# Kernel optimization log

Measured on AMD Instinct MI355X. Metric: run time of the kernel, lower is better.

Reference implementation:

```python
import jax, jax.numpy as jnp
import numpy as np

DENOM = 1.0 * (32 ** 0.5)  # temperature * map_rank**0.5
LN_EPS = 1e-5


def setup_inputs() -> dict:
    key = jax.random.key(0)
    ks = jax.random.split(key, 12)
    B, S, SC, MC, R, O = 4, 512, 128, 64, 32, 64
    sc = lambda *sh: 1.0 / np.sqrt(sh[0])
    return {
        "map_": jax.random.normal(ks[0], (B, MC, S, S), jnp.float32),
        "seq": jax.random.normal(ks[1], (B, S, SC), jnp.float32),
        "Wq": jax.random.normal(ks[2], (SC, R), jnp.float32) * sc(SC),
        "bq": jax.random.normal(ks[3], (R,), jnp.float32) * 0.01,
        "Wk": jax.random.normal(ks[4], (SC, R), jnp.float32) * sc(SC),
        "bk": jax.random.normal(ks[5], (R,), jnp.float32) * 0.01,
        "Wv": jax.random.normal(ks[6], (MC, MC), jnp.float32) * sc(MC),
        "bv": jax.random.normal(ks[7], (MC,), jnp.float32) * 0.01,
        "gamma": jnp.ones((MC,), jnp.float32),
        "beta": jnp.zeros((MC,), jnp.float32),
        "W1": jax.random.normal(ks[8], (MC, 4 * O), jnp.float32) * sc(MC),
        "b1": jax.random.normal(ks[9], (4 * O,), jnp.float32) * 0.01,
        "W2": jax.random.normal(ks[10], (4 * O, O), jnp.float32) * sc(4 * O),
        "b2": jax.random.normal(ks[11], (O,), jnp.float32) * 0.01,
    }


def _layernorm(x, gamma, beta):
    mu = jnp.mean(x, axis=-1, keepdims=True)
    var = jnp.mean(jnp.square(x - mu), axis=-1, keepdims=True)
    return (x - mu) * jax.lax.rsqrt(var + LN_EPS) * gamma + beta


def reference(map_, seq, Wq, bq, Wk, bk, Wv, bv, gamma, beta, W1, b1, W2, b2):
    q = seq @ Wq + bq                                   # [B,S,R]
    k = seq @ Wk + bk                                   # [B,S,R]
    v = jnp.einsum('bcst,cd->bstd', map_, Wv) + bv      # [B,S,S,C] (permute(0,2,3,1) @ Wv)
    logits = jnp.einsum('bsr,btr->bst', q, k) / DENOM   # [B,S,S]
    attn = jax.nn.softmax(logits, axis=2)
    pooled = jnp.einsum('bst,bstc->bsc', attn, v)       # weighted sum over dim 2
    score = _layernorm(pooled, gamma, beta)             # [B,S,C]
    h = jax.nn.relu(score @ W1 + b1)                    # MLP hidden [B,S,4*O]
    return h @ W2 + b2                                  # [B,S,O]
```

## Files before the change

### kernel.cpp

```cpp
#include <hip/hip_runtime.h>

#define NB 4
#define NS 512
#define NSC 128
#define NMC 64
#define NR 32
#define NO 64
#define NHID 256

__device__ __forceinline__ float wave_sum(float v) {
    #pragma unroll
    for (int m = 1; m < 64; m <<= 1) v += __shfl_xor(v, m, 64);
    return v;
}
__device__ __forceinline__ float wave_max(float v) {
    #pragma unroll
    for (int m = 1; m < 64; m <<= 1) v = fmaxf(v, __shfl_xor(v, m, 64));
    return v;
}

__global__ __launch_bounds__(64) void qk_kernel(
    const float* __restrict__ seq,
    const float* __restrict__ Wq, const float* __restrict__ bq,
    const float* __restrict__ Wk, const float* __restrict__ bk,
    float* __restrict__ q, float* __restrict__ k) {
    int bs  = blockIdx.x;
    int tid = threadIdx.x;
    __shared__ float srow[NSC];
    const float* sp = seq + (size_t)bs * NSC;
    srow[tid]      = sp[tid];
    srow[tid + 64] = sp[tid + 64];
    __syncthreads();
    int r = tid & 31;
    const float* W    = (tid < 32) ? Wq : Wk;
    const float* bias = (tid < 32) ? bq : bk;
    float acc = bias[r];
    #pragma unroll 8
    for (int c = 0; c < NSC; ++c) acc += srow[c] * W[c * NR + r];
    float* dst = (tid < 32) ? q : k;
    dst[(size_t)bs * NR + r] = acc;
}

__global__ __launch_bounds__(256) void main_kernel(
    const float* __restrict__ map_,
    const float* __restrict__ q, const float* __restrict__ k,
    const float* __restrict__ Wv, const float* __restrict__ bv,
    const float* __restrict__ gamma, const float* __restrict__ beta,
    const float* __restrict__ W1, const float* __restrict__ b1,
    const float* __restrict__ W2, const float* __restrict__ b2,
    float* __restrict__ out) {
    const float DENOM_INV = 0.17677669529663687f;
    const float LN_EPS = 1e-5f;

    int bs   = blockIdx.x;
    int b    = bs >> 9;
    int s    = bs & 511;
    int tid  = threadIdx.x;
    int lane = tid & 63;
    int wave = tid >> 6;

    __shared__ float s_q[NR];
    __shared__ float s_attn[NS];
    __shared__ float s_red[8];
    __shared__ float s_m[NMC];
    __shared__ float s_score[NMC];
    __shared__ float s_h[NHID];

    if (tid < NR) s_q[tid] = q[(size_t)bs * NR + tid];
    __syncthreads();

    const float* kb = k + (size_t)b * NS * NR;
    float lg0, lg1;
    {
        const float* kr0 = kb + (size_t)tid * NR;
        const float* kr1 = kb + (size_t)(tid + 256) * NR;
        float a0 = 0.f, a1 = 0.f;
        #pragma unroll
        for (int r = 0; r < NR; ++r) {
            a0 += s_q[r] * kr0[r];
            a1 += s_q[r] * kr1[r];
        }
        lg0 = a0 * DENOM_INV;
        lg1 = a1 * DENOM_INV;
    }

    float mx = wave_max(fmaxf(lg0, lg1));
    if (lane == 0) s_red[wave] = mx;
    __syncthreads();
    mx = fmaxf(fmaxf(s_red[0], s_red[1]), fmaxf(s_red[2], s_red[3]));
    float e0 = expf(lg0 - mx), e1 = expf(lg1 - mx);
    float ssum = wave_sum(e0 + e1);
    if (lane == 0) s_red[4 + wave] = ssum;
    __syncthreads();
    float inv = 1.f / (s_red[4] + s_red[5] + s_red[6] + s_red[7]);
    s_attn[tid]       = e0 * inv;
    s_attn[tid + 256] = e1 * inv;
    __syncthreads();

    const float4* attn4 = (const float4*)s_attn;
    float4 w0 = attn4[lane];
    float4 w1 = attn4[lane + 64];
    for (int d = wave; d < NMC; d += 4) {
        const float4* mp4 = (const float4*)(map_ + (((size_t)b * NMC + d) * NS + s) * NS);
        float4 a0 = mp4[lane];
        float4 a1 = mp4[lane + 64];
        float acc = a0.x * w0.x + a0.y * w0.y + a0.z * w0.z + a0.w * w0.w
                  + a1.x * w1.x + a1.y * w1.y + a1.z * w1.z + a1.w * w1.w;
        acc = wave_sum(acc);
        if (lane == 0) s_m[d] = acc;
    }
    __syncthreads();

    if (tid < NMC) {
        float pooled = bv[tid];
        #pragma unroll 8
        for (int d = 0; d < NMC; ++d) pooled += s_m[d] * Wv[d * NMC + tid];
        float sum   = wave_sum(pooled);
        float sumsq = wave_sum(pooled * pooled);
        float mu  = sum * (1.f / NMC);
        float var = sumsq * (1.f / NMC) - mu * mu;
        float rsig = rsqrtf(var + LN_EPS);
        s_score[tid] = (pooled - mu) * rsig * gamma[tid] + beta[tid];
    }
    __syncthreads();

    {
        float hacc = b1[tid];
        #pragma unroll 8
        for (int c = 0; c < NMC; ++c) hacc += s_score[c] * W1[c * NHID + tid];
        s_h[tid] = fmaxf(hacc, 0.f);
    }
    __syncthreads();

    if (tid < NO) {
        float oacc = b2[tid];
        #pragma unroll 8
        for (int j = 0; j < NHID; ++j) oacc += s_h[j] * W2[j * NO + tid];
        out[(size_t)bs * NO + tid] = oacc;
    }
}

extern "C" void kernel_launch(void* const* d_in, const int* in_sizes, int n_in,
                              void* d_out, int out_size, void* d_ws, size_t ws_size,
                              hipStream_t stream) {
    const float* map_  = (const float*)d_in[0];
    const float* seq   = (const float*)d_in[1];
    const float* Wq    = (const float*)d_in[2];
    const float* bq    = (const float*)d_in[3];
    const float* Wk    = (const float*)d_in[4];
    const float* bk    = (const float*)d_in[5];
    const float* Wv    = (const float*)d_in[6];
    const float* bv    = (const float*)d_in[7];
    const float* gamma = (const float*)d_in[8];
    const float* beta  = (const float*)d_in[9];
    const float* W1    = (const float*)d_in[10];
    const float* b1    = (const float*)d_in[11];
    const float* W2    = (const float*)d_in[12];
    const float* b2    = (const float*)d_in[13];
    float* out = (float*)d_out;

    float* q = (float*)d_ws;
    float* kk = q + (size_t)NB * NS * NR;

    qk_kernel<<<NB * NS, 64, 0, stream>>>(seq, Wq, bq, Wk, bk, q, kk);
    main_kernel<<<NB * NS, 256, 0, stream>>>(map_, q, kk, Wv, bv, gamma, beta,
                                             W1, b1, W2, b2, out);
}
```

Measured before the change: 73.05 us.

## Replace per-channel wave reductions with shared-memory partial sums and unrolled map loads

Each wave now handles a contiguous block of 16 channels with a fully unrolled loop, so many global loads can be in flight at once. Per-lane partial dot products go to a padded shared array, and 64 threads each reduce one channel, replacing a 6-step shuffle reduction per channel. The softmax normalization is folded into the register weights, which removes one barrier, and the q·k dot product uses float4 loads. The cost is a larger shared buffer, reused for score/h, and a serial 64-element sum per thread.

```diff
diff --git a/kernel.cpp b/kernel.cpp
--- a/kernel.cpp
+++ b/kernel.cpp
@@ -63,8 +63,11 @@
     __shared__ float s_attn[NS];
     __shared__ float s_red[8];
     __shared__ float s_m[NMC];
-    __shared__ float s_score[NMC];
-    __shared__ float s_h[NHID];
+    __shared__ float s_part[NMC][65];
+
+    float* s_flat  = &s_part[0][0];
+    float* s_score = s_flat;
+    float* s_h     = s_flat + 64;
 
     if (tid < NR) s_q[tid] = q[(size_t)bs * NR + tid];
     __syncthreads();
@@ -72,13 +75,15 @@
     const float* kb = k + (size_t)b * NS * NR;
     float lg0, lg1;
     {
-        const float* kr0 = kb + (size_t)tid * NR;
-        const float* kr1 = kb + (size_t)(tid + 256) * NR;
+        const float4* q4 = (const float4*)s_q;
+        const float4* k0 = (const float4*)(kb + (size_t)tid * NR);
+        const float4* k1 = (const float4*)(kb + (size_t)(tid + 256) * NR);
         float a0 = 0.f, a1 = 0.f;
         #pragma unroll
-        for (int r = 0; r < NR; ++r) {
-            a0 += s_q[r] * kr0[r];
-            a1 += s_q[r] * kr1[r];
+        for (int r4 = 0; r4 < NR / 4; ++r4) {
+            float4 qv = q4[r4], kv0 = k0[r4], kv1 = k1[r4];
+            a0 += qv.x * kv0.x + qv.y * kv0.y + qv.z * kv0.z + qv.w * kv0.w;
+            a1 += qv.x * kv1.x + qv.y * kv1.y + qv.z * kv1.z + qv.w * kv1.w;
         }
         lg0 = a0 * DENOM_INV;
         lg1 = a1 * DENOM_INV;
@@ -89,25 +94,40 @@
     __syncthreads();
     mx = fmaxf(fmaxf(s_red[0], s_red[1]), fmaxf(s_red[2], s_red[3]));
     float e0 = expf(lg0 - mx), e1 = expf(lg1 - mx);
+    s_attn[tid]       = e0;
+    s_attn[tid + 256] = e1;
     float ssum = wave_sum(e0 + e1);
     if (lane == 0) s_red[4 + wave] = ssum;
     __syncthreads();
     float inv = 1.f / (s_red[4] + s_red[5] + s_red[6] + s_red[7]);
-    s_attn[tid]       = e0 * inv;
-    s_attn[tid + 256] = e1 * inv;
-    __syncthreads();
 
     const float4* attn4 = (const float4*)s_attn;
     float4 w0 = attn4[lane];
     float4 w1 = attn4[lane + 64];
-    for (int d = wave; d < NMC; d += 4) {
-        const float4* mp4 = (const float4*)(map_ + (((size_t)b * NMC + d) * NS + s) * NS);
-        float4 a0 = mp4[lane];
-        float4 a1 = mp4[lane + 64];
-        float acc = a0.x * w0.x + a0.y * w0.y + a0.z * w0.z + a0.w * w0.w
-                  + a1.x * w1.x + a1.y * w1.y + a1.z * w1.z + a1.w * w1.w;
-        acc = wave_sum(acc);
-        if (lane == 0) s_m[d] = acc;
+    w0.x *= inv; w0.y *= inv; w0.z *= inv; w0.w *= inv;
+    w1.x *= inv; w1.y *= inv; w1.z *= inv; w1.w *= inv;
+
+    {
+        int d0 = wave * 16;
+        const float4* base =
+            (const float4*)(map_ + (((size_t)b * NMC + d0) * NS + s) * NS);
+        #pragma unroll
+        for (int i = 0; i < 16; ++i) {
+            const float4* rp = base + (size_t)i * (NS * NS / 4);
+            float4 a0 = rp[lane];
+            float4 a1 = rp[lane + 64];
+            float acc = a0.x * w0.x + a0.y * w0.y + a0.z * w0.z + a0.w * w0.w
+                      + a1.x * w1.x + a1.y * w1.y + a1.z * w1.z + a1.w * w1.w;
+            s_part[d0 + i][lane] = acc;
+        }
+    }
+    __syncthreads();
+
+    if (tid < NMC) {
+        float acc = 0.f;
+        #pragma unroll 8
+        for (int i = 0; i < 64; ++i) acc += s_part[tid][i];
+        s_m[tid] = acc;
     }
     __syncthreads();
 
```

Result: faster. 69.76 us (-4.5%).

## Split fused kernel into attention, pooling, and tail kernels for parallelism

Applied to the files above, without the earlier changes.

The single fused kernel is split into separate attention-softmax, map-pooling, and MLP-tail kernels. The pooling kernel launches four times as many blocks, each handling 16 channels with nontemporal vector loads and a shared-memory reduction in place of per-channel wave shuffles. The tail kernel spreads the Wv and W2 matvecs across all 256 threads with partial sums. The aim is more memory-level parallelism on the 256MB map stream, at the cost of extra launches and a 4MB attention round-trip through global memory.

```diff
diff --git a/kernel.cpp b/kernel.cpp
--- a/kernel.cpp
+++ b/kernel.cpp
@@ -7,6 +7,8 @@
 #define NR 32
 #define NO 64
 #define NHID 256
+
+typedef float f4 __attribute__((ext_vector_type(4)));
 
 __device__ __forceinline__ float wave_sum(float v) {
     #pragma unroll
@@ -41,80 +43,121 @@
     dst[(size_t)bs * NR + r] = acc;
 }
 
-__global__ __launch_bounds__(256) void main_kernel(
-    const float* __restrict__ map_,
+__global__ __launch_bounds__(256) void attn_kernel(
     const float* __restrict__ q, const float* __restrict__ k,
+    float* __restrict__ attn) {
+    const float DENOM_INV = 0.17677669529663687f;
+    int bs   = blockIdx.x;
+    int b    = bs >> 9;
+    int tid  = threadIdx.x;
+    int lane = tid & 63;
+    int wave = tid >> 6;
+
+    __shared__ float s_q[NR];
+    __shared__ float s_red[8];
+    if (tid < NR) s_q[tid] = q[(size_t)bs * NR + tid];
+    __syncthreads();
+
+    const float* kb = k + (size_t)b * NS * NR;
+    const f4* q4 = (const f4*)s_q;
+    const f4* k0 = (const f4*)(kb + (size_t)tid * NR);
+    const f4* k1 = (const f4*)(kb + (size_t)(tid + 256) * NR);
+    float a0 = 0.f, a1 = 0.f;
+    #pragma unroll
+    for (int r4 = 0; r4 < NR / 4; ++r4) {
+        f4 qv = q4[r4], kv0 = k0[r4], kv1 = k1[r4];
+        a0 += qv.x * kv0.x + qv.y * kv0.y + qv.z * kv0.z + qv.w * kv0.w;
+        a1 += qv.x * kv1.x + qv.y * kv1.y + qv.z * kv1.z + qv.w * kv1.w;
+    }
+    float lg0 = a0 * DENOM_INV, lg1 = a1 * DENOM_INV;
+
+    float mx = wave_max(fmaxf(lg0, lg1));
+    if (lane == 0) s_red[wave] = mx;
+    __syncthreads();
+    mx = fmaxf(fmaxf(s_red[0], s_red[1]), fmaxf(s_red[2], s_red[3]));
+    float e0 = expf(lg0 - mx), e1 = expf(lg1 - mx);
+    float ssum = wave_sum(e0 + e1);
+    if (lane == 0) s_red[4 + wave] = ssum;
+    __syncthreads();
+    float inv = 1.f / (s_red[4] + s_red[5] + s_red[6] + s_red[7]);
+    float* ap = attn + (size_t)bs * NS;
+    ap[tid]       = e0 * inv;
+    ap[tid + 256] = e1 * inv;
+}
+
+__global__ __launch_bounds__(256) void pool_kernel(
+    const float* __restrict__ map_, const float* __restrict__ attn,
+    float* __restrict__ m) {
+    int bid  = blockIdx.x;
+    int bs   = bid & 2047;
+    int dblk = bid >> 11;
+    int b    = bs >> 9;
+    int s    = bs & 511;
+    int tid  = threadIdx.x;
+    int lane = tid & 63;
+    int wave = tid >> 6;
+
+    __shared__ float s_part[16][65];
+
+    const f4* attn4 = (const f4*)(attn + (size_t)bs * NS);
+    f4 w0 = attn4[lane];
+    f4 w1 = attn4[lane + 64];
+
+    int d0 = dblk * 16 + wave * 4;
+    const f4* base = (const f4*)(map_ + (((size_t)b * NMC + d0) * NS + s) * NS);
+    #pragma unroll
+    for (int i = 0; i < 4; ++i) {
+        const f4* rp = base + (size_t)i * (NS * NS / 4);
+        f4 a0 = __builtin_nontemporal_load(rp + lane);
+        f4 a1 = __builtin_nontemporal_load(rp + lane + 64);
+        float acc0 = a0.x * w0.x + a0.y * w0.y + a0.z * w0.z + a0.w * w0.w;
+        float acc1 = a1.x * w1.x + a1.y * w1.y + a1.z * w1.z + a1.w * w1.w;
+        s_part[wave * 4 + i][lane] = acc0 + acc1;
+    }
+    __syncthreads();
+
+    if (tid < 16) {
+        float acc = 0.f;
+        #pragma unroll 8
+        for (int j = 0; j < 64; ++j) acc += s_part[tid][j];
+        m[(size_t)bs * NMC + dblk * 16 + tid] = acc;
+    }
+}
+
+__global__ __launch_bounds__(256) void tail_kernel(
+    const float* __restrict__ m,
     const float* __restrict__ Wv, const float* __restrict__ bv,
     const float* __restrict__ gamma, const float* __restrict__ beta,
     const float* __restrict__ W1, const float* __restrict__ b1,
     const float* __restrict__ W2, const float* __restrict__ b2,
     float* __restrict__ out) {
-    const float DENOM_INV = 0.17677669529663687f;
     const float LN_EPS = 1e-5f;
-
-    int bs   = blockIdx.x;
-    int b    = bs >> 9;
-    int s    = bs & 511;
-    int tid  = threadIdx.x;
-    int lane = tid & 63;
-    int wave = tid >> 6;
-
-    __shared__ float s_q[NR];
-    __shared__ float s_attn[NS];
-    __shared__ float s_red[8];
+    int bs  = blockIdx.x;
+    int tid = threadIdx.x;
+    int c    = tid & 63;
+    int part = tid >> 6;
+
     __shared__ float s_m[NMC];
     __shared__ float s_score[NMC];
     __shared__ float s_h[NHID];
-
-    if (tid < NR) s_q[tid] = q[(size_t)bs * NR + tid];
-    __syncthreads();
-
-    const float* kb = k + (size_t)b * NS * NR;
-    float lg0, lg1;
+    __shared__ float s_p[4][65];
+
+    if (tid < NMC) s_m[tid] = m[(size_t)bs * NMC + tid];
+    __syncthreads();
+
     {
-        const float* kr0 = kb + (size_t)tid * NR;
-        const float* kr1 = kb + (size_t)(tid + 256) * NR;
-        float a0 = 0.f, a1 = 0.f;
+        float acc = 0.f;
         #pragma unroll
-        for (int r = 0; r < NR; ++r) {
-            a0 += s_q[r] * kr0[r];
-            a1 += s_q[r] * kr1[r];
+        for (int i = 0; i < 16; ++i) {
+            int d = part * 16 + i;
+            acc += s_m[d] * Wv[d * NMC + c];
         }
-        lg0 = a0 * DENOM_INV;
-        lg1 = a1 * DENOM_INV;
-    }
-
-    float mx = wave_max(fmaxf(lg0, lg1));
-    if (lane == 0) s_red[wave] = mx;
-    __syncthreads();
-    mx = fmaxf(fmaxf(s_red[0], s_red[1]), fmaxf(s_red[2], s_red[3]));
-    float e0 = expf(lg0 - mx), e1 = expf(lg1 - mx);
-    float ssum = wave_sum(e0 + e1);
-    if (lane == 0) s_red[4 + wave] = ssum;
-    __syncthreads();
-    float inv = 1.f / (s_red[4] + s_red[5] + s_red[6] + s_red[7]);
-    s_attn[tid]       = e0 * inv;
-    s_attn[tid + 256] = e1 * inv;
-    __syncthreads();
-
-    const float4* attn4 = (const float4*)s_attn;
-    float4 w0 = attn4[lane];
-    float4 w1 = attn4[lane + 64];
-    for (int d = wave; d < NMC; d += 4) {
-        const float4* mp4 = (const float4*)(map_ + (((size_t)b * NMC + d) * NS + s) * NS);
-        float4 a0 = mp4[lane];
-        float4 a1 = mp4[lane + 64];
-        float acc = a0.x * w0.x + a0.y * w0.y + a0.z * w0.z + a0.w * w0.w
-                  + a1.x * w1.x + a1.y * w1.y + a1.z * w1.z + a1.w * w1.w;
-        acc = wave_sum(acc);
-        if (lane == 0) s_m[d] = acc;
+        s_p[part][c] = acc;
     }
     __syncthreads();
 
     if (tid < NMC) {
-        float pooled = bv[tid];
-        #pragma unroll 8
-        for (int d = 0; d < NMC; ++d) pooled += s_m[d] * Wv[d * NMC + tid];
+        float pooled = bv[tid] + s_p[0][tid] + s_p[1][tid] + s_p[2][tid] + s_p[3][tid];
         float sum   = wave_sum(pooled);
         float sumsq = wave_sum(pooled * pooled);
         float mu  = sum * (1.f / NMC);
@@ -127,17 +170,25 @@
     {
         float hacc = b1[tid];
         #pragma unroll 8
-        for (int c = 0; c < NMC; ++c) hacc += s_score[c] * W1[c * NHID + tid];
+        for (int cc = 0; cc < NMC; ++cc) hacc += s_score[cc] * W1[cc * NHID + tid];
         s_h[tid] = fmaxf(hacc, 0.f);
     }
     __syncthreads();
 
-    if (tid < NO) {
-        float oacc = b2[tid];
-        #pragma unroll 8
-        for (int j = 0; j < NHID; ++j) oacc += s_h[j] * W2[j * NO + tid];
-        out[(size_t)bs * NO + tid] = oacc;
-    }
+    {
+        float acc = 0.f;
+        #pragma unroll
+        for (int i = 0; i < 64; ++i) {
+            int j = part * 64 + i;
+            acc += s_h[j] * W2[j * NO + c];
+        }
+        s_p[part][c] = acc;
+    }
+    __syncthreads();
+
+    if (tid < NO)
+        out[(size_t)bs * NO + tid] =
+            b2[tid] + s_p[0][tid] + s_p[1][tid] + s_p[2][tid] + s_p[3][tid];
 }
 
 extern "C" void kernel_launch(void* const* d_in, const int* in_sizes, int n_in,
@@ -159,10 +210,14 @@
     const float* b2    = (const float*)d_in[13];
     float* out = (float*)d_out;
 
-    float* q = (float*)d_ws;
-    float* kk = q + (size_t)NB * NS * NR;
-
-    qk_kernel<<<NB * NS, 64, 0, stream>>>(seq, Wq, bq, Wk, bk, q, kk);
-    main_kernel<<<NB * NS, 256, 0, stream>>>(map_, q, kk, Wv, bv, gamma, beta,
-                                             W1, b1, W2, b2, out);
-}
+    float* q    = (float*)d_ws;
+    float* kk   = q    + (size_t)NB * NS * NR;
+    float* attn = kk   + (size_t)NB * NS * NR;
+    float* m    = attn + (size_t)NB * NS * NS;
+
+    qk_kernel  <<<NB * NS,     64, 0, stream>>>(seq, Wq, bq, Wk, bk, q, kk);
+    attn_kernel<<<NB * NS,    256, 0, stream>>>(q, kk, attn);
+    pool_kernel<<<NB * NS * 4, 256, 0, stream>>>(map_, attn, m);
+    tail_kernel<<<NB * NS,    256, 0, stream>>>(m, Wv, bv, gamma, beta,
+                                                W1, b1, W2, b2, out);
+}
```

Measured after the change: 83.62 us. 1.14x slower.

## Prefetch map rows before softmax and widen block to 512 threads

Applied to the files above, without the earlier changes.

Block size doubles to 512 threads. Each wave issues loads for its 8 map channels up front, half of them before the logits/softmax phase, so global memory latency overlaps the attention computation. Per-lane partial dot products are reduced through a padded shared-memory transpose instead of per-channel wave shuffles. The Wv and W2 matvecs are split across all waves and reduced afterwards. This adds register pressure from holding 16 float4 values per thread, plus extra barriers.

```diff
diff --git a/kernel.cpp b/kernel.cpp
--- a/kernel.cpp
+++ b/kernel.cpp
@@ -7,6 +7,9 @@
 #define NR 32
 #define NO 64
 #define NHID 256
+#define SSQ (NS * NS)
+
+typedef float f4 __attribute__((ext_vector_type(4)));
 
 __device__ __forceinline__ float wave_sum(float v) {
     #pragma unroll
@@ -17,6 +20,10 @@
     #pragma unroll
     for (int m = 1; m < 64; m <<= 1) v = fmaxf(v, __shfl_xor(v, m, 64));
     return v;
+}
+__device__ __forceinline__ float dot4(f4 a0, f4 a1, f4 w0, f4 w1) {
+    return a0.x * w0.x + a0.y * w0.y + a0.z * w0.z + a0.w * w0.w
+         + a1.x * w1.x + a1.y * w1.y + a1.z * w1.z + a1.w * w1.w;
 }
 
 __global__ __launch_bounds__(64) void qk_kernel(
@@ -41,7 +48,7 @@
     dst[(size_t)bs * NR + r] = acc;
 }
 
-__global__ __launch_bounds__(256) void main_kernel(
+__global__ __launch_bounds__(512, 4) void fused_kernel(
     const float* __restrict__ map_,
     const float* __restrict__ q, const float* __restrict__ k,
     const float* __restrict__ Wv, const float* __restrict__ bv,
@@ -61,60 +68,98 @@
 
     __shared__ float s_q[NR];
     __shared__ float s_attn[NS];
-    __shared__ float s_red[8];
+    __shared__ float s_red[16];
+    __shared__ float s_part[NMC][65];
     __shared__ float s_m[NMC];
     __shared__ float s_score[NMC];
     __shared__ float s_h[NHID];
+    __shared__ float s_p[8][65];
+
+    int d0 = wave * 8;
+    const f4* base = (const f4*)(map_ + (((size_t)b * NMC + d0) * NS + s) * NS);
+    f4 x0 = base[lane + 0 * (SSQ / 4)], y0 = base[lane + 64 + 0 * (SSQ / 4)];
+    f4 x1 = base[lane + 1 * (SSQ / 4)], y1 = base[lane + 64 + 1 * (SSQ / 4)];
+    f4 x2 = base[lane + 2 * (SSQ / 4)], y2 = base[lane + 64 + 2 * (SSQ / 4)];
+    f4 x3 = base[lane + 3 * (SSQ / 4)], y3 = base[lane + 64 + 3 * (SSQ / 4)];
 
     if (tid < NR) s_q[tid] = q[(size_t)bs * NR + tid];
     __syncthreads();
-
-    const float* kb = k + (size_t)b * NS * NR;
-    float lg0, lg1;
-    {
-        const float* kr0 = kb + (size_t)tid * NR;
-        const float* kr1 = kb + (size_t)(tid + 256) * NR;
-        float a0 = 0.f, a1 = 0.f;
-        #pragma unroll
-        for (int r = 0; r < NR; ++r) {
-            a0 += s_q[r] * kr0[r];
-            a1 += s_q[r] * kr1[r];
+    {
+        const f4* q4 = (const f4*)s_q;
+        const f4* kr = (const f4*)(k + ((size_t)b * NS + tid) * NR);
+        float a = 0.f;
+        #pragma unroll
+        for (int r4 = 0; r4 < NR / 4; ++r4) {
+            f4 qv = q4[r4], kv = kr[r4];
+            a += qv.x * kv.x + qv.y * kv.y + qv.z * kv.z + qv.w * kv.w;
         }
-        lg0 = a0 * DENOM_INV;
-        lg1 = a1 * DENOM_INV;
-    }
-
-    float mx = wave_max(fmaxf(lg0, lg1));
-    if (lane == 0) s_red[wave] = mx;
-    __syncthreads();
-    mx = fmaxf(fmaxf(s_red[0], s_red[1]), fmaxf(s_red[2], s_red[3]));
-    float e0 = expf(lg0 - mx), e1 = expf(lg1 - mx);
-    float ssum = wave_sum(e0 + e1);
-    if (lane == 0) s_red[4 + wave] = ssum;
-    __syncthreads();
-    float inv = 1.f / (s_red[4] + s_red[5] + s_red[6] + s_red[7]);
-    s_attn[tid]       = e0 * inv;
-    s_attn[tid + 256] = e1 * inv;
-    __syncthreads();
-
-    const float4* attn4 = (const float4*)s_attn;
-    float4 w0 = attn4[lane];
-    float4 w1 = attn4[lane + 64];
-    for (int d = wave; d < NMC; d += 4) {
-        const float4* mp4 = (const float4*)(map_ + (((size_t)b * NMC + d) * NS + s) * NS);
-        float4 a0 = mp4[lane];
-        float4 a1 = mp4[lane + 64];
-        float acc = a0.x * w0.x + a0.y * w0.y + a0.z * w0.z + a0.w * w0.w
-                  + a1.x * w1.x + a1.y * w1.y + a1.z * w1.z + a1.w * w1.w;
-        acc = wave_sum(acc);
-        if (lane == 0) s_m[d] = acc;
+        float lg = a * DENOM_INV;
+        float mx = wave_max(lg);
+        if (lane == 0) s_red[wave] = mx;
+        __syncthreads();
+        mx = s_red[0];
+        #pragma unroll
+        for (int j = 1; j < 8; ++j) mx = fmaxf(mx, s_red[j]);
+        float e = expf(lg - mx);
+        float se = wave_sum(e);
+        if (lane == 0) s_red[8 + wave] = se;
+        __syncthreads();
+        float tot = s_red[8];
+        #pragma unroll
+        for (int j = 1; j < 8; ++j) tot += s_red[8 + j];
+        s_attn[tid] = e * (1.f / tot);
+    }
+    __syncthreads();
+
+    const f4* attn4 = (const f4*)s_attn;
+    f4 w0 = attn4[lane];
+    f4 w1 = attn4[lane + 64];
+
+    f4 x4 = base[lane + 4 * (SSQ / 4)], y4 = base[lane + 64 + 4 * (SSQ / 4)];
+    f4 x5 = base[lane + 5 * (SSQ / 4)], y5 = base[lane + 64 + 5 * (SSQ / 4)];
+    f4 x6 = base[lane + 6 * (SSQ / 4)], y6 = base[lane + 64 + 6 * (SSQ / 4)];
+    f4 x7 = base[lane + 7 * (SSQ / 4)], y7 = base[lane + 64 + 7 * (SSQ / 4)];
+
+    s_part[d0 + 0][lane] = dot4(x0, y0, w0, w1);
+    s_part[d0 + 1][lane] = dot4(x1, y1, w0, w1);
+    s_part[d0 + 2][lane] = dot4(x2, y2, w0, w1);
+    s_part[d0 + 3][lane] = dot4(x3, y3, w0, w1);
+    s_part[d0 + 4][lane] = dot4(x4, y4, w0, w1);
+    s_part[d0 + 5][lane] = dot4(x5, y5, w0, w1);
+    s_part[d0 + 6][lane] = dot4(x6, y6, w0, w1);
+    s_part[d0 + 7][lane] = dot4(x7, y7, w0, w1);
+    __syncthreads();
+
+    {
+        float r = 0.f;
+        #pragma unroll
+        for (int j = 0; j < 8; ++j) r += s_part[lane][wave * 8 + j];
+        s_p[wave][lane] = r;
+    }
+    __syncthreads();
+    if (tid < NMC) {
+        float mm = 0.f;
+        #pragma unroll
+        for (int j = 0; j < 8; ++j) mm += s_p[j][tid];
+        s_m[tid] = mm;
+    }
+    __syncthreads();
+
+    {
+        float acc = 0.f;
+        #pragma unroll
+        for (int i = 0; i < 8; ++i) {
+            int d = wave * 8 + i;
+            acc += s_m[d] * Wv[d * NMC + lane];
+        }
+        s_p[wave][lane] = acc;
     }
     __syncthreads();
 
     if (tid < NMC) {
         float pooled = bv[tid];
-        #pragma unroll 8
-        for (int d = 0; d < NMC; ++d) pooled += s_m[d] * Wv[d * NMC + tid];
+        #pragma unroll
+        for (int j = 0; j < 8; ++j) pooled += s_p[j][tid];
         float sum   = wave_sum(pooled);
         float sumsq = wave_sum(pooled * pooled);
         float mu  = sum * (1.f / NMC);
@@ -124,7 +169,7 @@
     }
     __syncthreads();
 
-    {
+    if (tid < NHID) {
         float hacc = b1[tid];
         #pragma unroll 8
         for (int c = 0; c < NMC; ++c) hacc += s_score[c] * W1[c * NHID + tid];
@@ -132,10 +177,21 @@
     }
     __syncthreads();
 
+    {
+        float acc = 0.f;
+        #pragma unroll
+        for (int i = 0; i < 32; ++i) {
+            int j = wave * 32 + i;
+            acc += s_h[j] * W2[j * NO + lane];
+        }
+        s_p[wave][lane] = acc;
+    }
+    __syncthreads();
+
     if (tid < NO) {
         float oacc = b2[tid];
-        #pragma unroll 8
-        for (int j = 0; j < NHID; ++j) oacc += s_h[j] * W2[j * NO + tid];
+        #pragma unroll
+        for (int j = 0; j < 8; ++j) oacc += s_p[j][tid];
         out[(size_t)bs * NO + tid] = oacc;
     }
 }
@@ -159,10 +215,10 @@
     const float* b2    = (const float*)d_in[13];
     float* out = (float*)d_out;
 
-    float* q = (float*)d_ws;
+    float* q  = (float*)d_ws;
     float* kk = q + (size_t)NB * NS * NR;
 
-    qk_kernel<<<NB * NS, 64, 0, stream>>>(seq, Wq, bq, Wk, bk, q, kk);
-    main_kernel<<<NB * NS, 256, 0, stream>>>(map_, q, kk, Wv, bv, gamma, beta,
-                                             W1, b1, W2, b2, out);
-}
+    qk_kernel   <<<NB * NS,  64, 0, stream>>>(seq, Wq, bq, Wk, bk, q, kk);
+    fused_kernel<<<NB * NS, 512, 0, stream>>>(map_, q, kk, Wv, bv, gamma, beta,
+                                              W1, b1, W2, b2, out);
+}
```

Result: slower. 77.91 us (+6.7%).
